# Performance work log

Hardware: AMD Instinct MI355X
Metric: run time of the kernel (lower is better)

The kernel has to match this reference:

```python
import jax, jax.numpy as jnp
import numpy as np

N_NODES = 50000


def _gcn_norm(edge_index, num_nodes):
    # add self loops, compute symmetric normalization D^-1/2 (A+I) D^-1/2
    loops = jnp.arange(num_nodes, dtype=edge_index.dtype)
    row = jnp.concatenate([edge_index[0], loops])
    col = jnp.concatenate([edge_index[1], loops])
    deg = jax.ops.segment_sum(jnp.ones_like(row, dtype=jnp.float32), col,
                              num_segments=num_nodes)
    dinv = jnp.where(deg > 0, jax.lax.rsqrt(deg), 0.0)
    norm = dinv[row] * dinv[col]  # [E']
    return row, col, norm


def _gcn_conv(x, W, b, row, col, norm, num_nodes):
    h = x @ W                       # [N, out] transform first (smaller dim)
    msg = h[row] * norm[:, None]    # gather along source nodes  [E', out]
    agg = jax.ops.segment_sum(msg, col, num_segments=num_nodes)  # scatter-add
    return agg + b


def setup_inputs() -> dict:
    key = jax.random.key(0)
    k1, k2, k3, k4 = jax.random.split(key, 4)
    x = jax.random.normal(k1, (N_NODES, 128), dtype=jnp.float32)
    edge_index = jax.random.randint(k2, (2, 800000), 0, N_NODES, dtype=jnp.int64)
    W1 = jax.random.normal(k3, (128, 128), dtype=jnp.float32) * (1.0 / np.sqrt(128))
    b1 = jnp.zeros((128,), dtype=jnp.float32)
    W2 = jax.random.normal(k4, (128, 16), dtype=jnp.float32) * (1.0 / np.sqrt(128))
    b2 = jnp.zeros((16,), dtype=jnp.float32)
    return {"x": x, "edge_index": edge_index, "W1": W1, "b1": b1, "W2": W2, "b2": b2}


def reference(x, edge_index, W1, b1, W2, b2):
    n = x.shape[0]
    row, col, norm = _gcn_norm(edge_index, n)
    h = _gcn_conv(x, W1, b1, row, col, norm, n)
    h = jax.nn.relu(h)
    h = _gcn_conv(h, W2, b2, row, col, norm, n)
    return jax.nn.log_softmax(h, axis=1)
```

## Files before the change

### kernel.cpp

```cpp
#include <hip/hip_runtime.h>
#include <math.h>

constexpr int N  = 50000;
constexpr int E  = 800000;
constexpr int F1 = 128;
constexpr int F2 = 16;
constexpr int BSHIFT  = 8;
constexpr int NBUCKET = (N + 255) >> BSHIFT;
constexpr int CHUNK   = 2048;
constexpr int CAP     = 6144;

typedef unsigned short ushort_t;
typedef unsigned char  uchar_t;
typedef __bf16 bf16x8 __attribute__((ext_vector_type(8)));
typedef float  f32x4  __attribute__((ext_vector_type(4)));

static __device__ __forceinline__ float blo(unsigned u) { return __uint_as_float(u << 16); }
static __device__ __forceinline__ float bhi(unsigned u) { return __uint_as_float(u & 0xffff0000u); }
static __device__ __forceinline__ ushort_t to_bf(float f) { __bf16 h = (__bf16)f; return *(ushort_t*)&h; }


__global__ __launch_bounds__(256) void k_scatterP(const int* __restrict__ row,
                                                  const int* __restrict__ col,
                                                  int* __restrict__ cursor,
                                                  unsigned* __restrict__ P,
                                                  const float* __restrict__ W1,
                                                  const float* __restrict__ W2,
                                                  const float* __restrict__ b1,
                                                  ushort_t* __restrict__ W1t,
                                                  ushort_t* __restrict__ W2t,
                                                  float* __restrict__ b1p) {
    __shared__ int hist[NBUCKET];
    __shared__ int cur[NBUCKET];
    int t = threadIdx.x;
    if (t < NBUCKET) hist[t] = 0;
    __syncthreads();
    int base = blockIdx.x * CHUNK;
#pragma unroll
    for (int i = 0; i < CHUNK / 256; ++i) {
        int e = base + i * 256 + t;
        if (e < E) atomicAdd(&hist[col[e] >> BSHIFT], 1);
    }
    __syncthreads();
    if (t < NBUCKET) cur[t] = t * CAP + atomicAdd(&cursor[t], hist[t]);
    __syncthreads();
#pragma unroll
    for (int i = 0; i < CHUNK / 256; ++i) {
        int e = base + i * 256 + t;
        if (e < E) {
            int c = col[e];
            int pos = atomicAdd(&cur[c >> BSHIFT], 1);
            P[pos] = ((unsigned)row[e] << BSHIFT) | (unsigned)(c & 255);
        }
    }

    int gi = blockIdx.x * 256 + t;
    if (gi < F1 * F1) {
        int k = gi >> 7, n = gi & 127;
        W1t[n * F1 + k] = to_bf(W1[gi]);
    }
    if (gi < F1 * F2) {
        int k = gi >> 4, n = gi & 15;
        int pk = (k & 15) * 8 + (k >> 4);
        W2t[n * F1 + pk] = to_bf(W2[gi]);
    }
    if (gi < F1) {
        b1p[(gi & 15) * 8 + (gi >> 4)] = b1[gi];
    }
}

__global__ __launch_bounds__(512) void k_binFinal(const unsigned* __restrict__ P,
                                                  const int* __restrict__ cursor,
                                                  ushort_t* __restrict__ csr16,
                                                  int* __restrict__ seg_start,
                                                  int* __restrict__ counts,
                                                  float* __restrict__ dinv) {
    __shared__ unsigned eb[CAP];
    __shared__ int cnt[256];
    __shared__ int cur[256];
    __shared__ int wtot[4];
    int t = threadIdx.x;
    int b = blockIdx.x;
    int lo = b << BSHIFT;
    int n_nodes = min(256, N - lo);
    int m = cursor[b];
    if (t < 256) cnt[t] = 0;
    __syncthreads();
    const unsigned* Pb = P + (size_t)b * CAP;
    for (int k = t; k < m; k += 512) {
        unsigned u = Pb[k];
        eb[k] = u;
        atomicAdd(&cnt[u & 255], 1);
    }
    __syncthreads();
    int lane = t & 63, wid = t >> 6;
    int v = 0, incl = 0;
    if (t < 256) {
        v = cnt[t];
        incl = v;
#pragma unroll
        for (int d = 1; d < 64; d <<= 1) {
            int u = __shfl_up(incl, d, 64);
            if (lane >= d) incl += u;
        }
        if (lane == 63) wtot[wid] = incl;
    }
    __syncthreads();
    if (t < 256) {
        int wb = 0;
        for (int w = 0; w < wid; ++w) wb += wtot[w];
        int o = b * CAP + wb + incl - v;
        cur[t] = o;
        if (t < n_nodes) {
            seg_start[lo + t] = o;
            counts[lo + t] = v;
            dinv[lo + t] = rsqrtf((float)v + 1.f);
        }
    }
    __syncthreads();
    for (int k = t; k < m; k += 512) {
        unsigned u = eb[k];
        int pos = atomicAdd(&cur[u & 255], 1);
        csr16[pos] = (ushort_t)(u >> BSHIFT);
    }
}

__global__ __launch_bounds__(256) void k_gemm1_mfma(const float* __restrict__ x,
                                                    const ushort_t* __restrict__ W1t,
                                                    const float* __restrict__ dinv,
                                                    uchar_t* __restrict__ h1q) {
    __shared__ ushort_t Wl[F1 * 136];
    int t = threadIdx.x;
    for (int i = t; i < F1 * 16; i += 256) {
        int n = i >> 4, c = (i & 15) * 8;
        *(int4*)&Wl[n * 136 + c] = *(const int4*)&W1t[n * F1 + c];
    }
    __syncthreads();

    int lane = t & 63, wv = t >> 6;
    int quad = lane >> 4, l15 = lane & 15;
    int arow = blockIdx.x * 64 + wv * 16 + l15;
    int rclamp = min(arow, N - 1);
    f32x4 acc[8] = {};

#pragma unroll
    for (int kk = 0; kk < 4; ++kk) {
        int k0 = kk * 32 + quad * 8;
        const float* xp = x + (size_t)rclamp * F1 + k0;
        float4 u0 = *(const float4*)xp;
        float4 u1 = *(const float4*)(xp + 4);
        bf16x8 a;
        a[0] = (__bf16)u0.x; a[1] = (__bf16)u0.y; a[2] = (__bf16)u0.z; a[3] = (__bf16)u0.w;
        a[4] = (__bf16)u1.x; a[5] = (__bf16)u1.y; a[6] = (__bf16)u1.z; a[7] = (__bf16)u1.w;
#pragma unroll
        for (int ct = 0; ct < 8; ++ct) {
            bf16x8 b = *(const bf16x8*)&Wl[(ct * 16 + l15) * 136 + k0];
            acc[ct] = __builtin_amdgcn_mfma_f32_16x16x32_bf16(a, b, acc[ct], 0, 0, 0);
        }
    }

    int orow0 = blockIdx.x * 64 + wv * 16 + quad * 4;
#pragma unroll
    for (int r = 0; r < 4; ++r) {
        int orow = orow0 + r;
        if (orow < N) {
            float d = dinv[orow];
            unsigned d0 = __builtin_amdgcn_cvt_pk_fp8_f32(acc[0][r] * d, acc[1][r] * d, 0, false);
            d0 = __builtin_amdgcn_cvt_pk_fp8_f32(acc[2][r] * d, acc[3][r] * d, d0, true);
            unsigned d1 = __builtin_amdgcn_cvt_pk_fp8_f32(acc[4][r] * d, acc[5][r] * d, 0, false);
            d1 = __builtin_amdgcn_cvt_pk_fp8_f32(acc[6][r] * d, acc[7][r] * d, d1, true);
            uint2 pw; pw.x = d0; pw.y = d1;
            *(uint2*)(h1q + (size_t)orow * F1 + l15 * 8) = pw;
        }
    }
}

__global__ __launch_bounds__(256) void k_gather1(const uchar_t* __restrict__ h1q,
                                                 const int* __restrict__ seg_start,
                                                 const int* __restrict__ counts,
                                                 const ushort_t* __restrict__ csr16,
                                                 const float* __restrict__ dinv,
                                                 const float* __restrict__ b1p,
                                                 ushort_t* __restrict__ h1rb) {
    int c = (blockIdx.x * 256 + threadIdx.x) >> 6;
    int lane = threadIdx.x & 63;
    if (c >= N) return;
    int sub = lane & 15, q = lane >> 4;
    int s = seg_start[c], e = s + counts[c];
    float acc[8] = {0.f, 0.f, 0.f, 0.f, 0.f, 0.f, 0.f, 0.f};
    for (int base = s; base < e; base += 4) {
        int k = base + q;
        bool valid = k < e;
        int r = c;
        if (valid) r = csr16[k];
        uint2 u = *(const uint2*)(h1q + (size_t)r * F1 + sub * 8);
        float w = valid ? 1.f : 0.f;
        acc[0] = fmaf(__builtin_amdgcn_cvt_f32_fp8(u.x, 0), w, acc[0]);
        acc[1] = fmaf(__builtin_amdgcn_cvt_f32_fp8(u.x, 1), w, acc[1]);
        acc[2] = fmaf(__builtin_amdgcn_cvt_f32_fp8(u.x, 2), w, acc[2]);
        acc[3] = fmaf(__builtin_amdgcn_cvt_f32_fp8(u.x, 3), w, acc[3]);
        acc[4] = fmaf(__builtin_amdgcn_cvt_f32_fp8(u.y, 0), w, acc[4]);
        acc[5] = fmaf(__builtin_amdgcn_cvt_f32_fp8(u.y, 1), w, acc[5]);
        acc[6] = fmaf(__builtin_amdgcn_cvt_f32_fp8(u.y, 2), w, acc[6]);
        acc[7] = fmaf(__builtin_amdgcn_cvt_f32_fp8(u.y, 3), w, acc[7]);
    }
    if (q == 0) {
        uint2 u = *(const uint2*)(h1q + (size_t)c * F1 + sub * 8);
        acc[0] += __builtin_amdgcn_cvt_f32_fp8(u.x, 0);
        acc[1] += __builtin_amdgcn_cvt_f32_fp8(u.x, 1);
        acc[2] += __builtin_amdgcn_cvt_f32_fp8(u.x, 2);
        acc[3] += __builtin_amdgcn_cvt_f32_fp8(u.x, 3);
        acc[4] += __builtin_amdgcn_cvt_f32_fp8(u.y, 0);
        acc[5] += __builtin_amdgcn_cvt_f32_fp8(u.y, 1);
        acc[6] += __builtin_amdgcn_cvt_f32_fp8(u.y, 2);
        acc[7] += __builtin_amdgcn_cvt_f32_fp8(u.y, 3);
    }
#pragma unroll
    for (int j = 0; j < 8; ++j) acc[j] += __shfl_xor(acc[j], 16);
#pragma unroll
    for (int j = 0; j < 8; ++j) acc[j] += __shfl_xor(acc[j], 32);
    if (q == 0) {
        float dc = dinv[c];
        float4 bb0 = ((const float4*)b1p)[sub * 2];
        float4 bb1 = ((const float4*)b1p)[sub * 2 + 1];
        float o0 = fmaxf(fmaf(dc, acc[0], bb0.x), 0.f);
        float o1 = fmaxf(fmaf(dc, acc[1], bb0.y), 0.f);
        float o2 = fmaxf(fmaf(dc, acc[2], bb0.z), 0.f);
        float o3 = fmaxf(fmaf(dc, acc[3], bb0.w), 0.f);
        float o4 = fmaxf(fmaf(dc, acc[4], bb1.x), 0.f);
        float o5 = fmaxf(fmaf(dc, acc[5], bb1.y), 0.f);
        float o6 = fmaxf(fmaf(dc, acc[6], bb1.z), 0.f);
        float o7 = fmaxf(fmaf(dc, acc[7], bb1.w), 0.f);
        int4 pw;
        pw.x = (int)((unsigned)to_bf(o0) | ((unsigned)to_bf(o1) << 16));
        pw.y = (int)((unsigned)to_bf(o2) | ((unsigned)to_bf(o3) << 16));
        pw.z = (int)((unsigned)to_bf(o4) | ((unsigned)to_bf(o5) << 16));
        pw.w = (int)((unsigned)to_bf(o6) | ((unsigned)to_bf(o7) << 16));
        *(int4*)(h1rb + (size_t)c * F1 + sub * 8) = pw;
    }
}

__global__ __launch_bounds__(256) void k_gemm2_mfma(const ushort_t* __restrict__ h1rb,
                                                    const ushort_t* __restrict__ W2t,
                                                    const float* __restrict__ dinv,
                                                    ushort_t* __restrict__ h2s) {
    int t = threadIdx.x, lane = t & 63, wv = t >> 6;
    int quad = lane >> 4, l15 = lane & 15;
    int arow = blockIdx.x * 64 + wv * 16 + l15;
    int rclamp = min(arow, N - 1);
    f32x4 acc = {};
#pragma unroll
    for (int kk = 0; kk < 4; ++kk) {
        int k0 = kk * 32 + quad * 8;
        bf16x8 a = *(const bf16x8*)(h1rb + (size_t)rclamp * F1 + k0);
        bf16x8 b = *(const bf16x8*)(W2t + l15 * F1 + k0);
        acc = __builtin_amdgcn_mfma_f32_16x16x32_bf16(a, b, acc, 0, 0, 0);
    }
    int orow0 = blockIdx.x * 64 + wv * 16 + quad * 4;
#pragma unroll
    for (int r = 0; r < 4; ++r) {
        int orow = orow0 + r;
        if (orow < N)
            h2s[(size_t)orow * F2 + l15] = to_bf(acc[r] * dinv[orow]);
    }
}

__global__ __launch_bounds__(256) void k_gather2(const ushort_t* __restrict__ h2s,
                                                 const int* __restrict__ seg_start,
                                                 const int* __restrict__ counts,
                                                 const ushort_t* __restrict__ csr16,
                                                 const float* __restrict__ dinv,
                                                 const float* __restrict__ b2,
                                                 float* __restrict__ out) {
    int idx = blockIdx.x * 256 + threadIdx.x;
    int node = idx >> 3, sub = idx & 7;
    if (node >= N) return;
    int s = seg_start[node], e = s + counts[node];
    float ax = 0.f, ay = 0.f;
    int k = s;
    for (; k + 4 <= e; k += 4) {
        int r0 = csr16[k], r1 = csr16[k + 1], r2 = csr16[k + 2], r3 = csr16[k + 3];
        unsigned u0 = ((const unsigned*)(h2s + (size_t)r0 * F2))[sub];
        unsigned u1 = ((const unsigned*)(h2s + (size_t)r1 * F2))[sub];
        unsigned u2 = ((const unsigned*)(h2s + (size_t)r2 * F2))[sub];
        unsigned u3 = ((const unsigned*)(h2s + (size_t)r3 * F2))[sub];
        ax += (blo(u0) + blo(u1)) + (blo(u2) + blo(u3));
        ay += (bhi(u0) + bhi(u1)) + (bhi(u2) + bhi(u3));
    }
    for (; k < e; ++k) {
        unsigned u = ((const unsigned*)(h2s + (size_t)csr16[k] * F2))[sub];
        ax += blo(u);
        ay += bhi(u);
    }
    unsigned us = ((const unsigned*)(h2s + (size_t)node * F2))[sub];
    ax += blo(us);
    ay += bhi(us);
    float dc = dinv[node];
    float2 bb = ((const float2*)b2)[sub];
    float v0 = fmaf(dc, ax, bb.x);
    float v1 = fmaf(dc, ay, bb.y);
    float mx = fmaxf(v0, v1);
#pragma unroll
    for (int m = 1; m < 8; m <<= 1) mx = fmaxf(mx, __shfl_xor(mx, m));
    float sm = expf(v0 - mx) + expf(v1 - mx);
#pragma unroll
    for (int m = 1; m < 8; m <<= 1) sm += __shfl_xor(sm, m);
    float lse = mx + logf(sm);
    float2 o;
    o.x = v0 - lse;
    o.y = v1 - lse;
    ((float2*)(out + (size_t)node * F2))[sub] = o;
}

extern "C" void kernel_launch(void* const* d_in, const int* in_sizes, int n_in,
                              void* d_out, int out_size, void* d_ws, size_t ws_size,
                              hipStream_t stream) {
    const float* x  = (const float*)d_in[0];
    const int*   ei = (const int*)d_in[1];
    const float* W1 = (const float*)d_in[2];
    const float* b1 = (const float*)d_in[3];
    const float* W2 = (const float*)d_in[4];
    const float* b2 = (const float*)d_in[5];
    const int* row = ei;
    const int* col = ei + E;

    char* ws = (char*)d_ws;
    int*      cursor    = (int*)ws;      ws += 256 * 4;
    unsigned* P         = (unsigned*)ws; ws += (size_t)NBUCKET * CAP * 4;
    ushort_t* csr16     = (ushort_t*)ws; ws += (size_t)(NBUCKET * CAP + 8) * 2;
    int*      seg_start = (int*)ws;      ws += (size_t)N * 4;
    int*      counts    = (int*)ws;      ws += (size_t)N * 4;
    float*    dinv      = (float*)ws;    ws += (size_t)N * 4;
    float*    b1p       = (float*)ws;    ws += (size_t)F1 * 4;
    ushort_t* W1t       = (ushort_t*)ws; ws += (size_t)F1 * F1 * 2;
    ushort_t* W2t       = (ushort_t*)ws; ws += (size_t)F2 * F1 * 2;
    uchar_t*  h1q       = (uchar_t*)ws;  ws += (size_t)N * F1;
    ushort_t* h1rb      = (ushort_t*)ws; ws += (size_t)N * F1 * 2;
    ushort_t* h2s       = (ushort_t*)ws; ws += (size_t)N * F2 * 2;

    hipMemsetAsync(cursor, 0, 256 * 4, stream);

    int nbin_blocks = (E + CHUNK - 1) / CHUNK;
    k_scatterP<<<nbin_blocks, 256, 0, stream>>>(row, col, cursor, P, W1, W2, b1, W1t, W2t, b1p);
    k_binFinal<<<NBUCKET, 512, 0, stream>>>(P, cursor, csr16, seg_start, counts, dinv);

    k_gemm1_mfma<<<(N + 63) / 64, 256, 0, stream>>>(x, W1t, dinv, h1q);
    k_gather1<<<((size_t)N * 64 + 255) / 256, 256, 0, stream>>>(h1q, seg_start, counts, csr16,
                                                                dinv, b1p, h1rb);

    k_gemm2_mfma<<<(N + 63) / 64, 256, 0, stream>>>(h1rb, W2t, dinv, h2s);
    k_gather2<<<((size_t)N * 8 + 255) / 256, 256, 0, stream>>>(h2s, seg_start, counts, csr16,
                                                               dinv, b2, (float*)d_out);
}
```

Baseline: 166.0 us.

## Fuse GEMM1 into edge scatter launch and GEMM2 into layer-1 gather

Merges the edge-bucketing kernel and the first dense transform into one launch, with separate block ranges doing independent work. Because the transform now runs before degrees are known, the source-side dinv scaling moves into the gather as a per-edge weight. The second layer's 128x16 transform is folded into the gather epilogue using shared memory and shuffles, which removes the bf16 h1 intermediate and two kernel launches. The cost is an extra dinv load per edge, and fp8 quantisation now happens on values that are not yet scaled by dinv, which may change precision.

```diff
diff --git a/kernel.cpp b/kernel.cpp
--- a/kernel.cpp
+++ b/kernel.cpp
@@ -8,6 +8,8 @@
 constexpr int BSHIFT  = 8;
 constexpr int NBUCKET = (N + 255) >> BSHIFT;
 constexpr int CHUNK   = 2048;
+constexpr int NB_S    = (E + CHUNK - 1) / CHUNK;
+constexpr int NB_G    = (N + 63) / 64;
 constexpr int CAP     = 6144;
 
 typedef unsigned short ushort_t;
@@ -20,52 +22,83 @@
 static __device__ __forceinline__ ushort_t to_bf(float f) { __bf16 h = (__bf16)f; return *(ushort_t*)&h; }
 
 
-__global__ __launch_bounds__(256) void k_scatterP(const int* __restrict__ row,
-                                                  const int* __restrict__ col,
-                                                  int* __restrict__ cursor,
-                                                  unsigned* __restrict__ P,
-                                                  const float* __restrict__ W1,
-                                                  const float* __restrict__ W2,
-                                                  const float* __restrict__ b1,
-                                                  ushort_t* __restrict__ W1t,
-                                                  ushort_t* __restrict__ W2t,
-                                                  float* __restrict__ b1p) {
-    __shared__ int hist[NBUCKET];
-    __shared__ int cur[NBUCKET];
+__global__ __launch_bounds__(256) void k_scatG1(const int* __restrict__ row,
+                                                const int* __restrict__ col,
+                                                int* __restrict__ cursor,
+                                                unsigned* __restrict__ P,
+                                                const float* __restrict__ W1,
+                                                const float* __restrict__ x,
+                                                uchar_t* __restrict__ h1q) {
+    __shared__ ushort_t smem[F1 * 136];
     int t = threadIdx.x;
-    if (t < NBUCKET) hist[t] = 0;
-    __syncthreads();
-    int base = blockIdx.x * CHUNK;
-#pragma unroll
-    for (int i = 0; i < CHUNK / 256; ++i) {
-        int e = base + i * 256 + t;
-        if (e < E) atomicAdd(&hist[col[e] >> BSHIFT], 1);
-    }
-    __syncthreads();
-    if (t < NBUCKET) cur[t] = t * CAP + atomicAdd(&cursor[t], hist[t]);
-    __syncthreads();
-#pragma unroll
-    for (int i = 0; i < CHUNK / 256; ++i) {
-        int e = base + i * 256 + t;
-        if (e < E) {
-            int c = col[e];
-            int pos = atomicAdd(&cur[c >> BSHIFT], 1);
-            P[pos] = ((unsigned)row[e] << BSHIFT) | (unsigned)(c & 255);
-        }
-    }
-
-    int gi = blockIdx.x * 256 + t;
-    if (gi < F1 * F1) {
-        int k = gi >> 7, n = gi & 127;
-        W1t[n * F1 + k] = to_bf(W1[gi]);
-    }
-    if (gi < F1 * F2) {
-        int k = gi >> 4, n = gi & 15;
-        int pk = (k & 15) * 8 + (k >> 4);
-        W2t[n * F1 + pk] = to_bf(W2[gi]);
-    }
-    if (gi < F1) {
-        b1p[(gi & 15) * 8 + (gi >> 4)] = b1[gi];
+
+    if (blockIdx.x < NB_S) {
+        int* hist = (int*)smem;
+        int* cur  = hist + NBUCKET;
+        if (t < NBUCKET) hist[t] = 0;
+        __syncthreads();
+        int base = blockIdx.x * CHUNK;
+#pragma unroll
+        for (int i = 0; i < CHUNK / 256; ++i) {
+            int e = base + i * 256 + t;
+            if (e < E) atomicAdd(&hist[col[e] >> BSHIFT], 1);
+        }
+        __syncthreads();
+        if (t < NBUCKET) cur[t] = t * CAP + atomicAdd(&cursor[t], hist[t]);
+        __syncthreads();
+#pragma unroll
+        for (int i = 0; i < CHUNK / 256; ++i) {
+            int e = base + i * 256 + t;
+            if (e < E) {
+                int c = col[e];
+                int pos = atomicAdd(&cur[c >> BSHIFT], 1);
+                P[pos] = ((unsigned)row[e] << BSHIFT) | (unsigned)(c & 255);
+            }
+        }
+        return;
+    }
+
+    int blk = blockIdx.x - NB_S;
+    for (int i = t; i < F1 * F1; i += 256) {
+        int k = i >> 7, n = i & 127;
+        smem[n * 136 + k] = to_bf(W1[i]);
+    }
+    __syncthreads();
+
+    int lane = t & 63, wv = t >> 6;
+    int quad = lane >> 4, l15 = lane & 15;
+    int arow = blk * 64 + wv * 16 + l15;
+    int rclamp = min(arow, N - 1);
+    f32x4 acc[8] = {};
+
+#pragma unroll
+    for (int kk = 0; kk < 4; ++kk) {
+        int k0 = kk * 32 + quad * 8;
+        const float* xp = x + (size_t)rclamp * F1 + k0;
+        float4 u0 = *(const float4*)xp;
+        float4 u1 = *(const float4*)(xp + 4);
+        bf16x8 a;
+        a[0] = (__bf16)u0.x; a[1] = (__bf16)u0.y; a[2] = (__bf16)u0.z; a[3] = (__bf16)u0.w;
+        a[4] = (__bf16)u1.x; a[5] = (__bf16)u1.y; a[6] = (__bf16)u1.z; a[7] = (__bf16)u1.w;
+#pragma unroll
+        for (int ct = 0; ct < 8; ++ct) {
+            bf16x8 b = *(const bf16x8*)&smem[(ct * 16 + l15) * 136 + k0];
+            acc[ct] = __builtin_amdgcn_mfma_f32_16x16x32_bf16(a, b, acc[ct], 0, 0, 0);
+        }
+    }
+
+    int orow0 = blk * 64 + wv * 16 + quad * 4;
+#pragma unroll
+    for (int r = 0; r < 4; ++r) {
+        int orow = orow0 + r;
+        if (orow < N) {
+            unsigned d0 = __builtin_amdgcn_cvt_pk_fp8_f32(acc[0][r], acc[1][r], 0, false);
+            d0 = __builtin_amdgcn_cvt_pk_fp8_f32(acc[2][r], acc[3][r], d0, true);
+            unsigned d1 = __builtin_amdgcn_cvt_pk_fp8_f32(acc[4][r], acc[5][r], 0, false);
+            d1 = __builtin_amdgcn_cvt_pk_fp8_f32(acc[6][r], acc[7][r], d1, true);
+            uint2 pw; pw.x = d0; pw.y = d1;
+            *(uint2*)(h1q + (size_t)orow * F1 + l15 * 8) = pw;
+        }
     }
 }
 
@@ -125,76 +158,31 @@
     }
 }
 
-__global__ __launch_bounds__(256) void k_gemm1_mfma(const float* __restrict__ x,
-                                                    const ushort_t* __restrict__ W1t,
-                                                    const float* __restrict__ dinv,
-                                                    uchar_t* __restrict__ h1q) {
-    __shared__ ushort_t Wl[F1 * 136];
-    int t = threadIdx.x;
-    for (int i = t; i < F1 * 16; i += 256) {
-        int n = i >> 4, c = (i & 15) * 8;
-        *(int4*)&Wl[n * 136 + c] = *(const int4*)&W1t[n * F1 + c];
-    }
-    __syncthreads();
-
-    int lane = t & 63, wv = t >> 6;
-    int quad = lane >> 4, l15 = lane & 15;
-    int arow = blockIdx.x * 64 + wv * 16 + l15;
-    int rclamp = min(arow, N - 1);
-    f32x4 acc[8] = {};
-
-#pragma unroll
-    for (int kk = 0; kk < 4; ++kk) {
-        int k0 = kk * 32 + quad * 8;
-        const float* xp = x + (size_t)rclamp * F1 + k0;
-        float4 u0 = *(const float4*)xp;
-        float4 u1 = *(const float4*)(xp + 4);
-        bf16x8 a;
-        a[0] = (__bf16)u0.x; a[1] = (__bf16)u0.y; a[2] = (__bf16)u0.z; a[3] = (__bf16)u0.w;
-        a[4] = (__bf16)u1.x; a[5] = (__bf16)u1.y; a[6] = (__bf16)u1.z; a[7] = (__bf16)u1.w;
-#pragma unroll
-        for (int ct = 0; ct < 8; ++ct) {
-            bf16x8 b = *(const bf16x8*)&Wl[(ct * 16 + l15) * 136 + k0];
-            acc[ct] = __builtin_amdgcn_mfma_f32_16x16x32_bf16(a, b, acc[ct], 0, 0, 0);
-        }
-    }
-
-    int orow0 = blockIdx.x * 64 + wv * 16 + quad * 4;
-#pragma unroll
-    for (int r = 0; r < 4; ++r) {
-        int orow = orow0 + r;
-        if (orow < N) {
-            float d = dinv[orow];
-            unsigned d0 = __builtin_amdgcn_cvt_pk_fp8_f32(acc[0][r] * d, acc[1][r] * d, 0, false);
-            d0 = __builtin_amdgcn_cvt_pk_fp8_f32(acc[2][r] * d, acc[3][r] * d, d0, true);
-            unsigned d1 = __builtin_amdgcn_cvt_pk_fp8_f32(acc[4][r] * d, acc[5][r] * d, 0, false);
-            d1 = __builtin_amdgcn_cvt_pk_fp8_f32(acc[6][r] * d, acc[7][r] * d, d1, true);
-            uint2 pw; pw.x = d0; pw.y = d1;
-            *(uint2*)(h1q + (size_t)orow * F1 + l15 * 8) = pw;
-        }
-    }
-}
-
 __global__ __launch_bounds__(256) void k_gather1(const uchar_t* __restrict__ h1q,
                                                  const int* __restrict__ seg_start,
                                                  const int* __restrict__ counts,
                                                  const ushort_t* __restrict__ csr16,
                                                  const float* __restrict__ dinv,
-                                                 const float* __restrict__ b1p,
-                                                 ushort_t* __restrict__ h1rb) {
-    int c = (blockIdx.x * 256 + threadIdx.x) >> 6;
-    int lane = threadIdx.x & 63;
-    if (c >= N) return;
+                                                 const float* __restrict__ b1,
+                                                 const float* __restrict__ W2,
+                                                 ushort_t* __restrict__ h2s) {
+    __shared__ float W2l[F1 * F2];
+    __shared__ float hr[4][F1];
+    int t = threadIdx.x;
+    for (int i = t; i < F1 * F2; i += 256) W2l[i] = W2[i];
+    __syncthreads();
+
+    int c = (blockIdx.x * 256 + t) >> 6;
+    int lane = t & 63, wv = t >> 6;
     int sub = lane & 15, q = lane >> 4;
     int s = seg_start[c], e = s + counts[c];
     float acc[8] = {0.f, 0.f, 0.f, 0.f, 0.f, 0.f, 0.f, 0.f};
     for (int base = s; base < e; base += 4) {
         int k = base + q;
         bool valid = k < e;
-        int r = c;
-        if (valid) r = csr16[k];
+        int r = valid ? (int)csr16[k] : c;
+        float w = valid ? dinv[r] : 0.f;
         uint2 u = *(const uint2*)(h1q + (size_t)r * F1 + sub * 8);
-        float w = valid ? 1.f : 0.f;
         acc[0] = fmaf(__builtin_amdgcn_cvt_f32_fp8(u.x, 0), w, acc[0]);
         acc[1] = fmaf(__builtin_amdgcn_cvt_f32_fp8(u.x, 1), w, acc[1]);
         acc[2] = fmaf(__builtin_amdgcn_cvt_f32_fp8(u.x, 2), w, acc[2]);
@@ -204,65 +192,39 @@
         acc[6] = fmaf(__builtin_amdgcn_cvt_f32_fp8(u.y, 2), w, acc[6]);
         acc[7] = fmaf(__builtin_amdgcn_cvt_f32_fp8(u.y, 3), w, acc[7]);
     }
+    float dc = dinv[c];
     if (q == 0) {
         uint2 u = *(const uint2*)(h1q + (size_t)c * F1 + sub * 8);
-        acc[0] += __builtin_amdgcn_cvt_f32_fp8(u.x, 0);
-        acc[1] += __builtin_amdgcn_cvt_f32_fp8(u.x, 1);
-        acc[2] += __builtin_amdgcn_cvt_f32_fp8(u.x, 2);
-        acc[3] += __builtin_amdgcn_cvt_f32_fp8(u.x, 3);
-        acc[4] += __builtin_amdgcn_cvt_f32_fp8(u.y, 0);
-        acc[5] += __builtin_amdgcn_cvt_f32_fp8(u.y, 1);
-        acc[6] += __builtin_amdgcn_cvt_f32_fp8(u.y, 2);
-        acc[7] += __builtin_amdgcn_cvt_f32_fp8(u.y, 3);
+        acc[0] = fmaf(__builtin_amdgcn_cvt_f32_fp8(u.x, 0), dc, acc[0]);
+        acc[1] = fmaf(__builtin_amdgcn_cvt_f32_fp8(u.x, 1), dc, acc[1]);
+        acc[2] = fmaf(__builtin_amdgcn_cvt_f32_fp8(u.x, 2), dc, acc[2]);
+        acc[3] = fmaf(__builtin_amdgcn_cvt_f32_fp8(u.x, 3), dc, acc[3]);
+        acc[4] = fmaf(__builtin_amdgcn_cvt_f32_fp8(u.y, 0), dc, acc[4]);
+        acc[5] = fmaf(__builtin_amdgcn_cvt_f32_fp8(u.y, 1), dc, acc[5]);
+        acc[6] = fmaf(__builtin_amdgcn_cvt_f32_fp8(u.y, 2), dc, acc[6]);
+        acc[7] = fmaf(__builtin_amdgcn_cvt_f32_fp8(u.y, 3), dc, acc[7]);
     }
 #pragma unroll
     for (int j = 0; j < 8; ++j) acc[j] += __shfl_xor(acc[j], 16);
 #pragma unroll
     for (int j = 0; j < 8; ++j) acc[j] += __shfl_xor(acc[j], 32);
     if (q == 0) {
-        float dc = dinv[c];
-        float4 bb0 = ((const float4*)b1p)[sub * 2];
-        float4 bb1 = ((const float4*)b1p)[sub * 2 + 1];
-        float o0 = fmaxf(fmaf(dc, acc[0], bb0.x), 0.f);
-        float o1 = fmaxf(fmaf(dc, acc[1], bb0.y), 0.f);
-        float o2 = fmaxf(fmaf(dc, acc[2], bb0.z), 0.f);
-        float o3 = fmaxf(fmaf(dc, acc[3], bb0.w), 0.f);
-        float o4 = fmaxf(fmaf(dc, acc[4], bb1.x), 0.f);
-        float o5 = fmaxf(fmaf(dc, acc[5], bb1.y), 0.f);
-        float o6 = fmaxf(fmaf(dc, acc[6], bb1.z), 0.f);
-        float o7 = fmaxf(fmaf(dc, acc[7], bb1.w), 0.f);
-        int4 pw;
-        pw.x = (int)((unsigned)to_bf(o0) | ((unsigned)to_bf(o1) << 16));
-        pw.y = (int)((unsigned)to_bf(o2) | ((unsigned)to_bf(o3) << 16));
-        pw.z = (int)((unsigned)to_bf(o4) | ((unsigned)to_bf(o5) << 16));
-        pw.w = (int)((unsigned)to_bf(o6) | ((unsigned)to_bf(o7) << 16));
-        *(int4*)(h1rb + (size_t)c * F1 + sub * 8) = pw;
-    }
-}
-
-__global__ __launch_bounds__(256) void k_gemm2_mfma(const ushort_t* __restrict__ h1rb,
-                                                    const ushort_t* __restrict__ W2t,
-                                                    const float* __restrict__ dinv,
-                                                    ushort_t* __restrict__ h2s) {
-    int t = threadIdx.x, lane = t & 63, wv = t >> 6;
-    int quad = lane >> 4, l15 = lane & 15;
-    int arow = blockIdx.x * 64 + wv * 16 + l15;
-    int rclamp = min(arow, N - 1);
-    f32x4 acc = {};
-#pragma unroll
-    for (int kk = 0; kk < 4; ++kk) {
-        int k0 = kk * 32 + quad * 8;
-        bf16x8 a = *(const bf16x8*)(h1rb + (size_t)rclamp * F1 + k0);
-        bf16x8 b = *(const bf16x8*)(W2t + l15 * F1 + k0);
-        acc = __builtin_amdgcn_mfma_f32_16x16x32_bf16(a, b, acc, 0, 0, 0);
-    }
-    int orow0 = blockIdx.x * 64 + wv * 16 + quad * 4;
-#pragma unroll
-    for (int r = 0; r < 4; ++r) {
-        int orow = orow0 + r;
-        if (orow < N)
-            h2s[(size_t)orow * F2 + l15] = to_bf(acc[r] * dinv[orow]);
-    }
+#pragma unroll
+        for (int j = 0; j < 8; ++j) {
+            float o = fmaxf(fmaf(dc, acc[j], b1[j * 16 + sub]), 0.f);
+            hr[wv][j * 16 + sub] = o;
+        }
+    }
+    float a2 = 0.f;
+#pragma unroll
+    for (int i = 0; i < 32; ++i) {
+        int k = q * 32 + i;
+        a2 = fmaf(hr[wv][k], W2l[k * 16 + sub], a2);
+    }
+    a2 += __shfl_xor(a2, 16);
+    a2 += __shfl_xor(a2, 32);
+    if (q == 0)
+        h2s[(size_t)c * F2 + sub] = to_bf(a2 * dc);
 }
 
 __global__ __launch_bounds__(256) void k_gather2(const ushort_t* __restrict__ h2s,
@@ -331,24 +293,15 @@
     int*      seg_start = (int*)ws;      ws += (size_t)N * 4;
     int*      counts    = (int*)ws;      ws += (size_t)N * 4;
     float*    dinv      = (float*)ws;    ws += (size_t)N * 4;
-    float*    b1p       = (float*)ws;    ws += (size_t)F1 * 4;
-    ushort_t* W1t       = (ushort_t*)ws; ws += (size_t)F1 * F1 * 2;
-    ushort_t* W2t       = (ushort_t*)ws; ws += (size_t)F2 * F1 * 2;
     uchar_t*  h1q       = (uchar_t*)ws;  ws += (size_t)N * F1;
-    ushort_t* h1rb      = (ushort_t*)ws; ws += (size_t)N * F1 * 2;
     ushort_t* h2s       = (ushort_t*)ws; ws += (size_t)N * F2 * 2;
 
     hipMemsetAsync(cursor, 0, 256 * 4, stream);
 
-    int nbin_blocks = (E + CHUNK - 1) / CHUNK;
-    k_scatterP<<<nbin_blocks, 256, 0, stream>>>(row, col, cursor, P, W1, W2, b1, W1t, W2t, b1p);
+    k_scatG1<<<NB_S + NB_G, 256, 0, stream>>>(row, col, cursor, P, W1, x, h1q);
     k_binFinal<<<NBUCKET, 512, 0, stream>>>(P, cursor, csr16, seg_start, counts, dinv);
-
-    k_gemm1_mfma<<<(N + 63) / 64, 256, 0, stream>>>(x, W1t, dinv, h1q);
-    k_gather1<<<((size_t)N * 64 + 255) / 256, 256, 0, stream>>>(h1q, seg_start, counts, csr16,
-                                                                dinv, b1p, h1rb);
-
-    k_gemm2_mfma<<<(N + 63) / 64, 256, 0, stream>>>(h1rb, W2t, dinv, h2s);
+    k_gather1<<<(N * 64) / 256, 256, 0, stream>>>(h1q, seg_start, counts, csr16, dinv, b1, W2,
+                                                  h2s);
     k_gather2<<<((size_t)N * 8 + 255) / 256, 256, 0, stream>>>(h2s, seg_start, counts, csr16,
                                                                dinv, b2, (float*)d_out);
 }
```

Result: slower. 171.5 us (+3.3%).
